# Kernel tuning notes

Measured on AMD Instinct MI355X. Metric: run time of the kernel, lower is better.

## Reference

```python
import jax, jax.numpy as jnp
import numpy as np

N, E, G = 50000, 800000, 1024
F_IN, GH, HEADS, MH = 128, 64, 4, 64
C1 = GH // 2  # 32 per-head channels in gat1


def _p(key, shape, scale=0.05):
    return (scale * jax.random.normal(key, shape)).astype(jnp.float32)


def setup_inputs() -> dict:
    key = jax.random.key(0)
    ks = jax.random.split(key, 24)
    x = jax.random.normal(ks[0], (N, F_IN), dtype=jnp.float32)
    edge_index = jax.random.randint(ks[1], (2, E), 0, N, dtype=jnp.int64)
    batch = jnp.sort(jax.random.randint(ks[2], (N,), 0, G, dtype=jnp.int64))
    return {
        "x": x, "edge_index": edge_index, "batch": batch,
        # node_proj
        "Wp": _p(ks[3], (F_IN, GH)), "bp": jnp.zeros((GH,), jnp.float32),
        # gat1: in GH, out C1 per head, 4 heads, concat
        "W1": _p(ks[4], (GH, HEADS * C1)), "as1": _p(ks[5], (HEADS, C1)),
        "ad1": _p(ks[6], (HEADS, C1)), "b1": jnp.zeros((HEADS * C1,), jnp.float32),
        # gat2: in HEADS*C1=128, out GH, 1 head, no concat
        "W2": _p(ks[7], (HEADS * C1, GH)), "as2": _p(ks[8], (1, GH)),
        "ad2": _p(ks[9], (1, GH)), "b2": jnp.zeros((GH,), jnp.float32),
        # mlp + heads
        "Wm1": _p(ks[10], (GH, MH)), "bm1": jnp.zeros((MH,), jnp.float32),
        "Wm2": _p(ks[11], (MH, MH)), "bm2": jnp.zeros((MH,), jnp.float32),
        "Wc": _p(ks[12], (MH, 1)), "bc": jnp.zeros((1,), jnp.float32),
        "Wr": _p(ks[13], (MH, 1)), "br": jnp.zeros((1,), jnp.float32),
        "Wv": _p(ks[14], (MH, 1)), "bv": jnp.zeros((1,), jnp.float32),
    }


def gat_conv(h, src, dst, W, att_src, att_dst, bias, heads, out_ch, concat):
    n = h.shape[0]
    xh = (h @ W).reshape(n, heads, out_ch)          # [N,H,C]
    a_s = jnp.einsum("nhc,hc->nh", xh, att_src)      # [N,H]
    a_d = jnp.einsum("nhc,hc->nh", xh, att_dst)
    e = jax.nn.leaky_relu(a_s[src] + a_d[dst], 0.2)  # [E,H]
    # segment softmax over incoming edges of each dst node
    m = jax.ops.segment_max(e, dst, num_segments=n)
    e = jnp.exp(e - m[dst])
    denom = jax.ops.segment_sum(e, dst, num_segments=n)
    alpha = e / (denom[dst] + 1e-16)                 # [E,H]
    msg = xh[src] * alpha[:, :, None]                # [E,H,C]
    out = jax.ops.segment_sum(msg, dst, num_segments=n)
    out = out.reshape(n, heads * out_ch) if concat else out.mean(axis=1)
    return out + bias


def reference(x, edge_index, batch, Wp, bp, W1, as1, ad1, b1, W2, as2, ad2, b2,
              Wm1, bm1, Wm2, bm2, Wc, bc, Wr, br, Wv, bv):
    n = x.shape[0]
    loops = jnp.arange(n, dtype=edge_index.dtype)
    src = jnp.concatenate([edge_index[0], loops])  # PyG add_self_loops=True
    dst = jnp.concatenate([edge_index[1], loops])

    h = jax.nn.relu(x @ Wp + bp)
    h = jax.nn.elu(gat_conv(h, src, dst, W1, as1, ad1, b1, HEADS, C1, True))
    h = jax.nn.elu(gat_conv(h, src, dst, W2, as2, ad2, b2, 1, GH, False))

    # global mean pool over graphs
    sums = jax.ops.segment_sum(h, batch, num_segments=G)
    cnts = jax.ops.segment_sum(jnp.ones((n,), h.dtype), batch, num_segments=G)
    hg = sums / jnp.maximum(cnts, 1.0)[:, None]      # [G, GH]

    z = jax.nn.relu(hg @ Wm1 + bm1)
    z = jax.nn.relu(z @ Wm2 + bm2)
    class_logit = (z @ Wc + bc)[:, 0]
    ret = (z @ Wr + br)[:, 0]
    vol = jax.nn.softplus((z @ Wv + bv)[:, 0])
    return class_logit, ret, vol
```

## Files before the change

### kernel.cpp

```cpp
#include <hip/hip_runtime.h>
#include <hip/hip_bf16.h>
#include <math.h>

#define F_IN 128
#define GH   64

typedef __attribute__((ext_vector_type(8))) short bf16x8;
typedef __attribute__((ext_vector_type(4))) float f32x4;

__device__ __forceinline__ void edge_sd(const int* __restrict__ ei, int E, int e, int& s, int& d) {
    if (e < E) { s = ei[e]; d = ei[E + e]; } else { s = d = e - E; }
}
__device__ __forceinline__ float leaky(float x) { return (x >= 0.f) ? x : 0.2f * x; }
__device__ __forceinline__ unsigned short f2bf(float f) {
    unsigned u = __float_as_uint(f);
    u += 0x7FFFu + ((u >> 16) & 1u);
    return (unsigned short)(u >> 16);
}
__device__ __forceinline__ float bflo(unsigned v) { return __uint_as_float(v << 16); }
__device__ __forceinline__ float bfhi(unsigned v) { return __uint_as_float(v & 0xFFFF0000u); }

template<int K, int M, bool RELU, int AIN, int OM>
__global__ __launch_bounds__(256) void gemm_mfma(
    const float* __restrict__ Xf, const unsigned short* __restrict__ Xb,
    const float* __restrict__ W, const float* __restrict__ Bias,
    float* __restrict__ Yf, unsigned short* __restrict__ Yb, int nrows)
{
    constexpr int KP = K + 8;
    __shared__ unsigned short Als[64 * KP];
    __shared__ unsigned short Wls[M * KP];
    const int t = threadIdx.x;
    const int base = blockIdx.x * 64;

    for (int i = t; i < K * M / 4; i += 256) {
        int k  = i / (M / 4);
        int m0 = (i % (M / 4)) * 4;
        float4 wv = ((const float4*)W)[i];
        Wls[(m0 + 0) * KP + k] = f2bf(wv.x);
        Wls[(m0 + 1) * KP + k] = f2bf(wv.y);
        Wls[(m0 + 2) * KP + k] = f2bf(wv.z);
        Wls[(m0 + 3) * KP + k] = f2bf(wv.w);
    }
    if (AIN == 0) {
        for (int i = t; i < 64 * K / 4; i += 256) {
            int r  = i / (K / 4);
            int c4 = (i % (K / 4)) * 4;
            int n = base + r;
            float4 v = make_float4(0.f, 0.f, 0.f, 0.f);
            if (n < nrows) v = ((const float4*)(Xf + (size_t)n * K))[c4 >> 2];
            ushort4 pk = make_ushort4(f2bf(v.x), f2bf(v.y), f2bf(v.z), f2bf(v.w));
            *(ushort4*)&Als[r * KP + c4] = pk;
        }
    } else {
        for (int i = t; i < 64 * K / 8; i += 256) {
            int r  = i / (K / 8);
            int c8 = (i % (K / 8)) * 8;
            int n = base + r;
            uint4 v = make_uint4(0, 0, 0, 0);
            if (n < nrows) v = ((const uint4*)(Xb + (size_t)n * K))[c8 >> 3];
            *(uint4*)&Als[r * KP + c8] = v;
        }
    }
    __syncthreads();

    const int w = t >> 6, l = t & 63;
    const int lr = l & 15, lg = l >> 4;
    constexpr int CT = M / 16;
    f32x4 acc[CT];
#pragma unroll
    for (int ct = 0; ct < CT; ct++) acc[ct] = (f32x4){0.f, 0.f, 0.f, 0.f};

    const unsigned short* arow = &Als[(w * 16 + lr) * KP + lg * 8];
#pragma unroll
    for (int ks = 0; ks < K / 32; ks++) {
        bf16x8 a = *(const bf16x8*)(arow + ks * 32);
#pragma unroll
        for (int ct = 0; ct < CT; ct++) {
            bf16x8 b = *(const bf16x8*)&Wls[(ct * 16 + lr) * KP + ks * 32 + lg * 8];
            acc[ct] = __builtin_amdgcn_mfma_f32_16x16x32_bf16(a, b, acc[ct], 0, 0, 0);
        }
    }

#pragma unroll
    for (int ct = 0; ct < CT; ct++) {
        int col = ct * 16 + lr;
        float bb = Bias ? Bias[col] : 0.f;
#pragma unroll
        for (int r = 0; r < 4; r++) {
            int gr = base + w * 16 + lg * 4 + r;
            if (gr < nrows) {
                float v = acc[ct][r] + bb;
                if (RELU) v = fmaxf(v, 0.f);
                if (OM == 0) Yf[(size_t)gr * M + col] = v;
                else         Yb[(size_t)gr * M + col] = f2bf(v);
            }
        }
    }
}

__global__ __launch_bounds__(256) void asad1_kernel(
    const unsigned short* __restrict__ xhb, const float* __restrict__ asw,
    const float* __restrict__ adw, float* __restrict__ as_n, float* __restrict__ ad_n, int N)
{
    const int t = threadIdx.x;
    const int node = blockIdx.x * 4 + (t >> 6);
    const int lane = t & 63;
    if (node >= N) return;
    unsigned u = ((const unsigned*)xhb)[(size_t)node * 64 + lane];
    float x0 = bflo(u), x1 = bfhi(u);
    int c0 = 2 * lane;
    float ps = x0 * asw[c0] + x1 * asw[c0 + 1];
    float pd = x0 * adw[c0] + x1 * adw[c0 + 1];
#pragma unroll
    for (int msk = 8; msk >= 1; msk >>= 1) {
        ps += __shfl_xor(ps, msk);
        pd += __shfl_xor(pd, msk);
    }
    if ((lane & 15) == 0) {
        as_n[node * 4 + (lane >> 4)] = ps;
        ad_n[node * 4 + (lane >> 4)] = pd;
    }
}

__global__ __launch_bounds__(256) void asad2_kernel(
    const unsigned short* __restrict__ xhb, const float* __restrict__ asw,
    const float* __restrict__ adw, float* __restrict__ as_n, float* __restrict__ ad_n, int N)
{
    const int t = threadIdx.x;
    const int node = blockIdx.x * 8 + (t >> 5);
    const int li = t & 31;
    if (node >= N) return;
    unsigned u = ((const unsigned*)xhb)[(size_t)node * 32 + li];
    float x0 = bflo(u), x1 = bfhi(u);
    int c0 = 2 * li;
    float ps = x0 * asw[c0] + x1 * asw[c0 + 1];
    float pd = x0 * adw[c0] + x1 * adw[c0 + 1];
#pragma unroll
    for (int msk = 16; msk >= 1; msk >>= 1) {
        ps += __shfl_xor(ps, msk);
        pd += __shfl_xor(pd, msk);
    }
    if (li == 0) { as_n[node] = ps; ad_n[node] = pd; }
}

__global__ __launch_bounds__(256) void bucket_hist(
    const int* __restrict__ ei, int E, int ET, int N, int* __restrict__ bcnt)
{
    __shared__ int h[256];
    h[threadIdx.x] = 0;
    __syncthreads();
    for (int e = blockIdx.x * 256 + threadIdx.x; e < ET; e += gridDim.x * 256) {
        int s, d; edge_sd(ei, E, e, s, d);
        if ((unsigned)s < (unsigned)N && (unsigned)d < (unsigned)N)
            atomicAdd(&h[d >> 8], 1);
    }
    __syncthreads();
    if (h[threadIdx.x]) atomicAdd(&bcnt[threadIdx.x], h[threadIdx.x]);
}

__global__ __launch_bounds__(256) void bucket_scan(
    const int* __restrict__ bcnt, int* __restrict__ bbase, int* __restrict__ bcur,
    int* __restrict__ row_start, int B, int N)
{
    __shared__ int wsum[4];
    int t = threadIdx.x, lane = t & 63, w = t >> 6;
    int v = (t < B) ? bcnt[t] : 0;
    int incl = v;
#pragma unroll
    for (int off = 1; off < 64; off <<= 1) {
        int n = __shfl_up(incl, off);
        if (lane >= off) incl += n;
    }
    if (lane == 63) wsum[w] = incl;
    __syncthreads();
    int wb = 0;
#pragma unroll
    for (int i = 0; i < 4; i++) if (i < w) wb += wsum[i];
    int excl = wb + incl - v;
    if (t < B) { bbase[t] = excl; bcur[t] = excl; }
    if (t == 255) { bbase[B] = excl + v; row_start[N] = excl + v; }
}

#define SCHUNK 4096
__global__ __launch_bounds__(256) void bucket_scatter(
    const int* __restrict__ ei, int E, int ET, int N,
    int* __restrict__ bcur, int* __restrict__ deg, uint2* __restrict__ staged)
{
    __shared__ int bc[256];
    __shared__ int bb[256];
    const int t = threadIdx.x;
    const int base = blockIdx.x * SCHUNK;
    bc[t] = 0;
    __syncthreads();
    const int cnt = min(SCHUNK, ET - base);
    int ss[16], dd[16], lr[16];
#pragma unroll
    for (int k = 0; k < 16; k++) {
        int i = t + k * 256;
        ss[k] = -1; dd[k] = 0; lr[k] = 0;
        if (i < cnt) {
            int s, d; edge_sd(ei, E, base + i, s, d);
            if ((unsigned)s < (unsigned)N && (unsigned)d < (unsigned)N) {
                ss[k] = s; dd[k] = d;
                lr[k] = atomicAdd(&bc[d >> 8], 1);
                atomicAdd(&deg[d], 1);
            }
        }
    }
    __syncthreads();
    bb[t] = bc[t] ? atomicAdd(&bcur[t], bc[t]) : 0;
    __syncthreads();
#pragma unroll
    for (int k = 0; k < 16; k++) {
        if (ss[k] >= 0)
            staged[bb[dd[k] >> 8] + lr[k]] = make_uint2((unsigned)ss[k], (unsigned)dd[k]);
    }
}

__global__ __launch_bounds__(256) void row_scan(
    const int* __restrict__ deg, const int* __restrict__ bbase,
    int* __restrict__ row_start, int N)
{
    __shared__ int wsum[4];
    const int b = blockIdx.x, t = threadIdx.x;
    const int lane = t & 63, w = t >> 6;
    const int node = b * 256 + t;
    int v = (node < N) ? deg[node] : 0;
    int incl = v;
#pragma unroll
    for (int off = 1; off < 64; off <<= 1) {
        int n = __shfl_up(incl, off);
        if (lane >= off) incl += n;
    }
    if (lane == 63) wsum[w] = incl;
    __syncthreads();
    int wb = 0;
#pragma unroll
    for (int i = 0; i < 4; i++) if (i < w) wb += wsum[i];
    if (node < N) row_start[node] = bbase[b] + wb + incl - v;
}

__global__ __launch_bounds__(256) void bucket_final(
    const uint2* __restrict__ staged, const int* __restrict__ bbase,
    const int* __restrict__ row_start, int* __restrict__ adj, int N)
{
    __shared__ int cur[256];
    const int b = blockIdx.x, t = threadIdx.x;
    const int node = b * 256 + t;
    cur[t] = (node < N) ? row_start[node] : 0;
    __syncthreads();
    const int beg = bbase[b], end = bbase[b + 1];
    for (int i = beg + t; i < end; i += 256) {
        uint2 sd = staged[i];
        int pos = atomicAdd(&cur[sd.y & 255], 1);
        adj[pos] = (int)sd.x;
    }
}

__global__ __launch_bounds__(256) void gat1_fused(
    const int* __restrict__ row_start, const int* __restrict__ adj,
    const float* __restrict__ as_n, const float* __restrict__ ad_n,
    const unsigned short* __restrict__ xhb, const float* __restrict__ b1,
    unsigned short* __restrict__ outb, int N)
{
    __shared__ unsigned s_ofs[4][64];
    __shared__ float    s_p[4][256];
    const int w = threadIdx.x >> 6;
    const int d = blockIdx.x * 4 + w;
    if (d >= N) return;
    const int lane = threadIdx.x & 63;
    const int h = lane >> 4;
    const int beg = row_start[d];
    const int deg = row_start[d + 1] - beg;
    const float4 adv = ((const float4*)ad_n)[d];
    const char* xbase = (const char*)xhb;

    float l0 = 0.f, l1 = 0.f, l2 = 0.f, l3 = 0.f;
    float acc0 = 0.f, acc1 = 0.f;
    for (int j0 = 0; j0 < deg; j0 += 64) {
        const int chunk = min(64, deg - j0);
        if (lane < chunk) {
            int s = adj[beg + j0 + lane];
            float4 asv = ((const float4*)as_n)[s];
            float p0 = __expf(leaky(asv.x + adv.x));
            float p1 = __expf(leaky(asv.y + adv.y));
            float p2 = __expf(leaky(asv.z + adv.z));
            float p3 = __expf(leaky(asv.w + adv.w));
            l0 += p0; l1 += p1; l2 += p2; l3 += p3;
            s_ofs[w][lane] = (unsigned)s << 8;
            ((float4*)&s_p[w][lane * 4])[0] = make_float4(p0, p1, p2, p3);
        }
        __threadfence_block();
#pragma unroll 4
        for (int jj = 0; jj < chunk; jj++) {
            float a = s_p[w][jj * 4 + h];
            unsigned ofs = s_ofs[w][jj] + ((unsigned)lane << 2);
            unsigned u = *(const unsigned*)(xbase + ofs);
            acc0 += a * bflo(u);
            acc1 += a * bfhi(u);
        }
        __threadfence_block();
    }
#pragma unroll
    for (int msk = 32; msk >= 1; msk >>= 1) {
        l0 += __shfl_xor(l0, msk); l1 += __shfl_xor(l1, msk);
        l2 += __shfl_xor(l2, msk); l3 += __shfl_xor(l3, msk);
    }
    float lh = (h == 0) ? l0 : (h == 1) ? l1 : (h == 2) ? l2 : l3;
    const float inv = 1.0f / (lh + 1e-16f);
    float2 bb = ((const float2*)b1)[lane];
    float v0 = acc0 * inv + bb.x;
    float v1 = acc1 * inv + bb.y;
    v0 = (v0 > 0.f) ? v0 : expm1f(v0);
    v1 = (v1 > 0.f) ? v1 : expm1f(v1);
    unsigned pk = (unsigned)f2bf(v0) | ((unsigned)f2bf(v1) << 16);
    ((unsigned*)outb)[(size_t)d * 64 + lane] = pk;
}

__global__ __launch_bounds__(256) void gat2_fused(
    const int* __restrict__ row_start, const int* __restrict__ adj,
    const float* __restrict__ as_n, const float* __restrict__ ad_n,
    const unsigned short* __restrict__ xhb, const float* __restrict__ b2,
    const int* __restrict__ batch, float* __restrict__ sums, float* __restrict__ cnts,
    int N, int G)
{
    __shared__ unsigned s_ofs[4][64];
    __shared__ float    s_p[4][64];
    __shared__ float    pbuf[4][64];
    __shared__ int      pg[4];
    const int w = threadIdx.x >> 6;
    const int d = blockIdx.x * 4 + w;
    const int lane = threadIdx.x & 63;
    const bool alive = (d < N);
    int beg = 0, deg = 0; float ad = 0.f; int g = -1;
    if (alive) {
        beg = row_start[d];
        deg = row_start[d + 1] - beg;
        ad = ad_n[d];
        int gb = batch[d];
        if ((unsigned)gb < (unsigned)G) g = gb;
    }
    const char* xbase = (const char*)xhb;
    float l = 0.f, acc = 0.f;
    for (int j0 = 0; j0 < deg; j0 += 64) {
        const int chunk = min(64, deg - j0);
        if (lane < chunk) {
            int s = adj[beg + j0 + lane];
            float p = __expf(leaky(as_n[s] + ad));
            l += p;
            s_ofs[w][lane] = (unsigned)s << 7;
            s_p[w][lane] = p;
        }
        __threadfence_block();
#pragma unroll 4
        for (int jj = 0; jj < chunk; jj++) {
            float a = s_p[w][jj];
            unsigned ofs = s_ofs[w][jj] + ((unsigned)lane << 1);
            unsigned short uv = *(const unsigned short*)(xbase + ofs);
            acc += a * __uint_as_float((unsigned)uv << 16);
        }
        __threadfence_block();
    }
#pragma unroll
    for (int msk = 32; msk >= 1; msk >>= 1) l += __shfl_xor(l, msk);
    float v = acc / (l + 1e-16f) + b2[lane];
    v = (v > 0.f) ? v : expm1f(v);

    if (lane == 0) pg[w] = g;
    pbuf[w][lane] = (g >= 0) ? v : 0.f;
    __syncthreads();
    int g0 = pg[0], g1 = pg[1], g2 = pg[2], g3 = pg[3];
    bool uni = (g0 >= 0) && (g1 == g0) && (g2 == g0) && (g3 == g0);
    if (uni) {
        if (w == 0) {
            float s4 = pbuf[0][lane] + pbuf[1][lane] + pbuf[2][lane] + pbuf[3][lane];
            atomicAdd(&sums[(size_t)g0 * 64 + lane], s4);
            if (lane == 0) atomicAdd(&cnts[g0], 4.0f);
        }
    } else if (g >= 0) {
        atomicAdd(&sums[(size_t)g * 64 + lane], v);
        if (lane == 0) atomicAdd(&cnts[g], 1.0f);
    }
}

__global__ __launch_bounds__(64) void mlp_head(
    const float* __restrict__ sums, const float* __restrict__ cnts,
    const float* __restrict__ Wm1, const float* __restrict__ bm1,
    const float* __restrict__ Wm2, const float* __restrict__ bm2,
    const float* __restrict__ Wc, const float* __restrict__ bc,
    const float* __restrict__ Wr, const float* __restrict__ br,
    const float* __restrict__ Wv, const float* __restrict__ bv,
    float* __restrict__ out, int G)
{
    int g = blockIdx.x;
    int t = threadIdx.x;
    __shared__ float hrow[64];
    __shared__ float zrow[64];
    float hv = sums[(size_t)g * 64 + t] / fmaxf(cnts[g], 1.0f);
    hrow[t] = hv;
    __syncthreads();
    float z1 = bm1[t];
#pragma unroll 8
    for (int k = 0; k < 64; k++) z1 += hrow[k] * Wm1[k * 64 + t];
    z1 = fmaxf(z1, 0.f);
    zrow[t] = z1;
    __syncthreads();
    float z2 = bm2[t];
#pragma unroll 8
    for (int k = 0; k < 64; k++) z2 += zrow[k] * Wm2[k * 64 + t];
    z2 = fmaxf(z2, 0.f);
    float pc = z2 * Wc[t], pr = z2 * Wr[t], pv = z2 * Wv[t];
#pragma unroll
    for (int m = 32; m >= 1; m >>= 1) {
        pc += __shfl_xor(pc, m);
        pr += __shfl_xor(pr, m);
        pv += __shfl_xor(pv, m);
    }
    if (t == 0) {
        out[g] = pc + bc[0];
        out[G + g] = pr + br[0];
        float s = pv + bv[0];
        out[2 * G + g] = (s > 20.f) ? s : log1pf(expf(s));
    }
}

extern "C" void kernel_launch(void* const* d_in, const int* in_sizes, int n_in,
                              void* d_out, int out_size, void* d_ws, size_t ws_size,
                              hipStream_t stream)
{
    const float* x     = (const float*)d_in[0];
    const int*   ei    = (const int*)d_in[1];
    const int*   batch = (const int*)d_in[2];
    const float* Wp  = (const float*)d_in[3];
    const float* bp  = (const float*)d_in[4];
    const float* W1  = (const float*)d_in[5];
    const float* as1 = (const float*)d_in[6];
    const float* ad1 = (const float*)d_in[7];
    const float* b1  = (const float*)d_in[8];
    const float* W2  = (const float*)d_in[9];
    const float* as2 = (const float*)d_in[10];
    const float* ad2 = (const float*)d_in[11];
    const float* b2  = (const float*)d_in[12];
    const float* Wm1 = (const float*)d_in[13];
    const float* bm1 = (const float*)d_in[14];
    const float* Wm2 = (const float*)d_in[15];
    const float* bm2 = (const float*)d_in[16];
    const float* Wc  = (const float*)d_in[17];
    const float* bc  = (const float*)d_in[18];
    const float* Wr  = (const float*)d_in[19];
    const float* br  = (const float*)d_in[20];
    const float* Wv  = (const float*)d_in[21];
    const float* bv  = (const float*)d_in[22];

    const int N  = in_sizes[0] / F_IN;
    const int E  = in_sizes[1] / 2;
    const int G  = out_size / 3;
    const int ET = E + N;
    const int B  = (N + 255) >> 8;

    float* ws = (float*)d_ws;
    size_t o = 0;
    unsigned short* h0b  = (unsigned short*)(ws + o); o += (size_t)N * 32;
    unsigned short* h1b  = (unsigned short*)(ws + o); o += (size_t)N * 64;
    unsigned short* xhb1 = (unsigned short*)(ws + o); o += (size_t)N * 64;
    unsigned short* xhb2 = (unsigned short*)(ws + o); o += (size_t)N * 32;
    float* as1n = ws + o; o += (size_t)N * 4;
    float* ad1n = ws + o; o += (size_t)N * 4;
    float* as2n = ws + o; o += (size_t)N;
    float* ad2n = ws + o; o += (size_t)N;
    int* row_start = (int*)(ws + o); o += (size_t)N + 1;
    int* adj       = (int*)(ws + o); o += (size_t)ET;
    int* bbase     = (int*)(ws + o); o += 257;
    int* bcur      = (int*)(ws + o); o += 256;
    uint2* staged  = (uint2*)(ws + o); o += (size_t)ET * 2;
    float* zstart = ws + o;
    int*   deg  = (int*)(ws + o); o += (size_t)N;
    int*   bcnt = (int*)(ws + o); o += 256;
    float* sums = ws + o;         o += (size_t)G * 64;
    float* cnts = ws + o;         o += (size_t)G;
    size_t zlen = (size_t)(ws + o - zstart) * sizeof(float);

    hipMemsetAsync(zstart, 0, zlen, stream);

    const int gN64 = (N + 63) / 64;
    const int gN4  = (N + 3) / 4;
    const int gSC  = (ET + SCHUNK - 1) / SCHUNK;

    bucket_hist<<<512, 256, 0, stream>>>(ei, E, ET, N, bcnt);
    bucket_scan<<<1, 256, 0, stream>>>(bcnt, bbase, bcur, row_start, B, N);
    bucket_scatter<<<gSC, 256, 0, stream>>>(ei, E, ET, N, bcur, deg, staged);
    row_scan<<<B, 256, 0, stream>>>(deg, bbase, row_start, N);
    bucket_final<<<B, 256, 0, stream>>>(staged, bbase, row_start, adj, N);

    gemm_mfma<128, 64, true, 0, 1><<<gN64, 256, 0, stream>>>(x, nullptr, Wp, bp, nullptr, h0b, N);
    gemm_mfma<64, 128, false, 1, 1><<<gN64, 256, 0, stream>>>(nullptr, h0b, W1, nullptr, nullptr, xhb1, N);
    asad1_kernel<<<gN4, 256, 0, stream>>>(xhb1, as1, ad1, as1n, ad1n, N);
    gat1_fused<<<gN4, 256, 0, stream>>>(row_start, adj, as1n, ad1n, xhb1, b1, h1b, N);
    gemm_mfma<128, 64, false, 1, 1><<<gN64, 256, 0, stream>>>(nullptr, h1b, W2, nullptr, nullptr, xhb2, N);
    asad2_kernel<<<(N + 7) / 8, 256, 0, stream>>>(xhb2, as2, ad2, as2n, ad2n, N);
    gat2_fused<<<gN4, 256, 0, stream>>>(row_start, adj, as2n, ad2n, xhb2, b2,
                                        batch, sums, cnts, N, G);
    mlp_head<<<G, 64, 0, stream>>>(sums, cnts, Wm1, bm1, Wm2, bm2,
                                   Wc, bc, Wr, br, Wv, bv, (float*)d_out, G);
}
```

Before: 331.6 us.

## Fuse attention dot products into GEMM epilogue and widen gather loads in GAT

```diff
diff --git a/kernel.cpp b/kernel.cpp
--- a/kernel.cpp
+++ b/kernel.cpp
@@ -20,11 +20,13 @@
 __device__ __forceinline__ float bflo(unsigned v) { return __uint_as_float(v << 16); }
 __device__ __forceinline__ float bfhi(unsigned v) { return __uint_as_float(v & 0xFFFF0000u); }
 
-template<int K, int M, bool RELU, int AIN, int OM>
+template<int K, int M, bool RELU, int AIN, int DOTS>
 __global__ __launch_bounds__(256) void gemm_mfma(
     const float* __restrict__ Xf, const unsigned short* __restrict__ Xb,
     const float* __restrict__ W, const float* __restrict__ Bias,
-    float* __restrict__ Yf, unsigned short* __restrict__ Yb, int nrows)
+    unsigned short* __restrict__ Yb,
+    const float* __restrict__ asw, const float* __restrict__ adw,
+    float* __restrict__ as_n, float* __restrict__ ad_n, int nrows)
 {
     constexpr int KP = K + 8;
     __shared__ unsigned short Als[64 * KP];
@@ -91,56 +93,78 @@
             if (gr < nrows) {
                 float v = acc[ct][r] + bb;
                 if (RELU) v = fmaxf(v, 0.f);
-                if (OM == 0) Yf[(size_t)gr * M + col] = v;
-                else         Yb[(size_t)gr * M + col] = f2bf(v);
-            }
-        }
-    }
-}
-
-__global__ __launch_bounds__(256) void asad1_kernel(
-    const unsigned short* __restrict__ xhb, const float* __restrict__ asw,
-    const float* __restrict__ adw, float* __restrict__ as_n, float* __restrict__ ad_n, int N)
-{
-    const int t = threadIdx.x;
-    const int node = blockIdx.x * 4 + (t >> 6);
-    const int lane = t & 63;
-    if (node >= N) return;
-    unsigned u = ((const unsigned*)xhb)[(size_t)node * 64 + lane];
-    float x0 = bflo(u), x1 = bfhi(u);
-    int c0 = 2 * lane;
-    float ps = x0 * asw[c0] + x1 * asw[c0 + 1];
-    float pd = x0 * adw[c0] + x1 * adw[c0 + 1];
-#pragma unroll
-    for (int msk = 8; msk >= 1; msk >>= 1) {
-        ps += __shfl_xor(ps, msk);
-        pd += __shfl_xor(pd, msk);
-    }
-    if ((lane & 15) == 0) {
-        as_n[node * 4 + (lane >> 4)] = ps;
-        ad_n[node * 4 + (lane >> 4)] = pd;
-    }
-}
-
-__global__ __launch_bounds__(256) void asad2_kernel(
-    const unsigned short* __restrict__ xhb, const float* __restrict__ asw,
-    const float* __restrict__ adw, float* __restrict__ as_n, float* __restrict__ ad_n, int N)
-{
-    const int t = threadIdx.x;
-    const int node = blockIdx.x * 8 + (t >> 5);
-    const int li = t & 31;
-    if (node >= N) return;
-    unsigned u = ((const unsigned*)xhb)[(size_t)node * 32 + li];
-    float x0 = bflo(u), x1 = bfhi(u);
-    int c0 = 2 * li;
-    float ps = x0 * asw[c0] + x1 * asw[c0 + 1];
-    float pd = x0 * adw[c0] + x1 * adw[c0 + 1];
-#pragma unroll
-    for (int msk = 16; msk >= 1; msk >>= 1) {
-        ps += __shfl_xor(ps, msk);
-        pd += __shfl_xor(pd, msk);
-    }
-    if (li == 0) { as_n[node] = ps; ad_n[node] = pd; }
+                Yb[(size_t)gr * M + col] = f2bf(v);
+            }
+        }
+    }
+
+    if (DOTS == 1) {
+        float hs[4][4], hd[4][4];
+#pragma unroll
+        for (int r = 0; r < 4; r++)
+#pragma unroll
+            for (int h = 0; h < 4; h++) { hs[r][h] = 0.f; hd[r][h] = 0.f; }
+#pragma unroll
+        for (int ct = 0; ct < CT; ct++) {
+            int col = ct * 16 + lr;
+            float aw = asw[col], dw = adw[col];
+            int h = ct >> 1;
+#pragma unroll
+            for (int r = 0; r < 4; r++) {
+                hs[r][h] += acc[ct][r] * aw;
+                hd[r][h] += acc[ct][r] * dw;
+            }
+        }
+#pragma unroll
+        for (int msk = 8; msk >= 1; msk >>= 1) {
+#pragma unroll
+            for (int r = 0; r < 4; r++)
+#pragma unroll
+                for (int h = 0; h < 4; h++) {
+                    hs[r][h] += __shfl_xor(hs[r][h], msk);
+                    hd[r][h] += __shfl_xor(hd[r][h], msk);
+                }
+        }
+        if (lr == 0) {
+#pragma unroll
+            for (int r = 0; r < 4; r++) {
+                int gr = base + w * 16 + lg * 4 + r;
+                if (gr < nrows) {
+                    ((float4*)as_n)[gr] = make_float4(hs[r][0], hs[r][1], hs[r][2], hs[r][3]);
+                    ((float4*)ad_n)[gr] = make_float4(hd[r][0], hd[r][1], hd[r][2], hd[r][3]);
+                }
+            }
+        }
+    } else if (DOTS == 2) {
+        float ps[4], pd[4];
+#pragma unroll
+        for (int r = 0; r < 4; r++) { ps[r] = 0.f; pd[r] = 0.f; }
+#pragma unroll
+        for (int ct = 0; ct < CT; ct++) {
+            int col = ct * 16 + lr;
+            float aw = asw[col], dw = adw[col];
+#pragma unroll
+            for (int r = 0; r < 4; r++) {
+                ps[r] += acc[ct][r] * aw;
+                pd[r] += acc[ct][r] * dw;
+            }
+        }
+#pragma unroll
+        for (int msk = 8; msk >= 1; msk >>= 1) {
+#pragma unroll
+            for (int r = 0; r < 4; r++) {
+                ps[r] += __shfl_xor(ps[r], msk);
+                pd[r] += __shfl_xor(pd[r], msk);
+            }
+        }
+        if (lr == 0) {
+#pragma unroll
+            for (int r = 0; r < 4; r++) {
+                int gr = base + w * 16 + lg * 4 + r;
+                if (gr < nrows) { as_n[gr] = ps[r]; ad_n[gr] = pd[r]; }
+            }
+        }
+    }
 }
 
 __global__ __launch_bounds__(256) void bucket_hist(
@@ -269,14 +293,16 @@
     const int d = blockIdx.x * 4 + w;
     if (d >= N) return;
     const int lane = threadIdx.x & 63;
-    const int h = lane >> 4;
+    const int li = lane & 31;
+    const int half = lane >> 5;
+    const int h = li >> 3;
     const int beg = row_start[d];
     const int deg = row_start[d + 1] - beg;
     const float4 adv = ((const float4*)ad_n)[d];
     const char* xbase = (const char*)xhb;
 
     float l0 = 0.f, l1 = 0.f, l2 = 0.f, l3 = 0.f;
-    float acc0 = 0.f, acc1 = 0.f;
+    float a0 = 0.f, a1 = 0.f, a2 = 0.f, a3 = 0.f;
     for (int j0 = 0; j0 < deg; j0 += 64) {
         const int chunk = min(64, deg - j0);
         if (lane < chunk) {
@@ -292,29 +318,38 @@
         }
         __threadfence_block();
 #pragma unroll 4
-        for (int jj = 0; jj < chunk; jj++) {
+        for (int jj = half; jj < chunk; jj += 2) {
             float a = s_p[w][jj * 4 + h];
-            unsigned ofs = s_ofs[w][jj] + ((unsigned)lane << 2);
-            unsigned u = *(const unsigned*)(xbase + ofs);
-            acc0 += a * bflo(u);
-            acc1 += a * bfhi(u);
+            unsigned ofs = s_ofs[w][jj] + ((unsigned)li << 3);
+            uint2 u = *(const uint2*)(xbase + ofs);
+            a0 += a * bflo(u.x); a1 += a * bfhi(u.x);
+            a2 += a * bflo(u.y); a3 += a * bfhi(u.y);
         }
         __threadfence_block();
     }
+    a0 += __shfl_xor(a0, 32); a1 += __shfl_xor(a1, 32);
+    a2 += __shfl_xor(a2, 32); a3 += __shfl_xor(a3, 32);
 #pragma unroll
     for (int msk = 32; msk >= 1; msk >>= 1) {
         l0 += __shfl_xor(l0, msk); l1 += __shfl_xor(l1, msk);
         l2 += __shfl_xor(l2, msk); l3 += __shfl_xor(l3, msk);
     }
-    float lh = (h == 0) ? l0 : (h == 1) ? l1 : (h == 2) ? l2 : l3;
-    const float inv = 1.0f / (lh + 1e-16f);
-    float2 bb = ((const float2*)b1)[lane];
-    float v0 = acc0 * inv + bb.x;
-    float v1 = acc1 * inv + bb.y;
-    v0 = (v0 > 0.f) ? v0 : expm1f(v0);
-    v1 = (v1 > 0.f) ? v1 : expm1f(v1);
-    unsigned pk = (unsigned)f2bf(v0) | ((unsigned)f2bf(v1) << 16);
-    ((unsigned*)outb)[(size_t)d * 64 + lane] = pk;
+    if (half == 0) {
+        float lh = (h == 0) ? l0 : (h == 1) ? l1 : (h == 2) ? l2 : l3;
+        const float inv = 1.0f / (lh + 1e-16f);
+        float4 bb = ((const float4*)b1)[li];
+        float v0 = a0 * inv + bb.x;
+        float v1 = a1 * inv + bb.y;
+        float v2 = a2 * inv + bb.z;
+        float v3 = a3 * inv + bb.w;
+        v0 = (v0 > 0.f) ? v0 : expm1f(v0);
+        v1 = (v1 > 0.f) ? v1 : expm1f(v1);
+        v2 = (v2 > 0.f) ? v2 : expm1f(v2);
+        v3 = (v3 > 0.f) ? v3 : expm1f(v3);
+        unsigned pk01 = (unsigned)f2bf(v0) | ((unsigned)f2bf(v1) << 16);
+        unsigned pk23 = (unsigned)f2bf(v2) | ((unsigned)f2bf(v3) << 16);
+        ((uint2*)((char*)outb + (size_t)d * 256))[li] = make_uint2(pk01, pk23);
+    }
 }
 
 __global__ __launch_bounds__(256) void gat2_fused(
@@ -331,6 +366,8 @@
     const int w = threadIdx.x >> 6;
     const int d = blockIdx.x * 4 + w;
     const int lane = threadIdx.x & 63;
+    const int li = lane & 31;
+    const int half = lane >> 5;
     const bool alive = (d < N);
     int beg = 0, deg = 0; float ad = 0.f; int g = -1;
     if (alive) {
@@ -341,7 +378,7 @@
         if ((unsigned)gb < (unsigned)G) g = gb;
     }
     const char* xbase = (const char*)xhb;
-    float l = 0.f, acc = 0.f;
+    float l = 0.f, a0 = 0.f, a1 = 0.f;
     for (int j0 = 0; j0 < deg; j0 += 64) {
         const int chunk = min(64, deg - j0);
         if (lane < chunk) {
@@ -353,21 +390,31 @@
         }
         __threadfence_block();
 #pragma unroll 4
-        for (int jj = 0; jj < chunk; jj++) {
+        for (int jj = half; jj < chunk; jj += 2) {
             float a = s_p[w][jj];
-            unsigned ofs = s_ofs[w][jj] + ((unsigned)lane << 1);
-            unsigned short uv = *(const unsigned short*)(xbase + ofs);
-            acc += a * __uint_as_float((unsigned)uv << 16);
+            unsigned ofs = s_ofs[w][jj] + ((unsigned)li << 2);
+            unsigned u = *(const unsigned*)(xbase + ofs);
+            a0 += a * bflo(u);
+            a1 += a * bfhi(u);
         }
         __threadfence_block();
     }
+    a0 += __shfl_xor(a0, 32);
+    a1 += __shfl_xor(a1, 32);
 #pragma unroll
     for (int msk = 32; msk >= 1; msk >>= 1) l += __shfl_xor(l, msk);
-    float v = acc / (l + 1e-16f) + b2[lane];
-    v = (v > 0.f) ? v : expm1f(v);
 
     if (lane == 0) pg[w] = g;
-    pbuf[w][lane] = (g >= 0) ? v : 0.f;
+    if (half == 0) {
+        const float inv = 1.0f / (l + 1e-16f);
+        float2 bb = ((const float2*)b2)[li];
+        float v0 = a0 * inv + bb.x;
+        float v1 = a1 * inv + bb.y;
+        v0 = (v0 > 0.f) ? v0 : expm1f(v0);
+        v1 = (v1 > 0.f) ? v1 : expm1f(v1);
+        ((float2*)&pbuf[w][2 * li])[0] = make_float2((g >= 0) ? v0 : 0.f,
+                                                    (g >= 0) ? v1 : 0.f);
+    }
     __syncthreads();
     int g0 = pg[0], g1 = pg[1], g2 = pg[2], g3 = pg[3];
     bool uni = (g0 >= 0) && (g1 == g0) && (g2 == g0) && (g3 == g0);
@@ -378,7 +425,7 @@
             if (lane == 0) atomicAdd(&cnts[g0], 4.0f);
         }
     } else if (g >= 0) {
-        atomicAdd(&sums[(size_t)g * 64 + lane], v);
+        atomicAdd(&sums[(size_t)g * 64 + lane], pbuf[w][lane]);
         if (lane == 0) atomicAdd(&cnts[g], 1.0f);
     }
 }
@@ -492,12 +539,13 @@
     row_scan<<<B, 256, 0, stream>>>(deg, bbase, row_start, N);
     bucket_final<<<B, 256, 0, stream>>>(staged, bbase, row_start, adj, N);
 
-    gemm_mfma<128, 64, true, 0, 1><<<gN64, 256, 0, stream>>>(x, nullptr, Wp, bp, nullptr, h0b, N);
-    gemm_mfma<64, 128, false, 1, 1><<<gN64, 256, 0, stream>>>(nullptr, h0b, W1, nullptr, nullptr, xhb1, N);
-    asad1_kernel<<<gN4, 256, 0, stream>>>(xhb1, as1, ad1, as1n, ad1n, N);
+    gemm_mfma<128, 64, true, 0, 0><<<gN64, 256, 0, stream>>>(
+        x, nullptr, Wp, bp, h0b, nullptr, nullptr, nullptr, nullptr, N);
+    gemm_mfma<64, 128, false, 1, 1><<<gN64, 256, 0, stream>>>(
+        nullptr, h0b, W1, nullptr, xhb1, as1, ad1, as1n, ad1n, N);
     gat1_fused<<<gN4, 256, 0, stream>>>(row_start, adj, as1n, ad1n, xhb1, b1, h1b, N);
-    gemm_mfma<128, 64, false, 1, 1><<<gN64, 256, 0, stream>>>(nullptr, h1b, W2, nullptr, nullptr, xhb2, N);
-    asad2_kernel<<<(N + 7) / 8, 256, 0, stream>>>(xhb2, as2, ad2, as2n, ad2n, N);
+    gemm_mfma<128, 64, false, 1, 2><<<gN64, 256, 0, stream>>>(
+        nullptr, h1b, W2, nullptr, xhb2, as2, ad2, as2n, ad2n, N);
     gat2_fused<<<gN4, 256, 0, stream>>>(row_start, adj, as2n, ad2n, xhb2, b2,
                                         batch, sums, cnts, N, G);
     mlp_head<<<G, 64, 0, stream>>>(sums, cnts, Wm1, bm1, Wm2, bm2,
```

Measured after the change: 321.2 us. 3.2% less time.
